# Performance work log

Hardware: AMD Instinct MI355X
Metric: run time of the kernel (lower is better)

The kernel has to match this reference:

```python
import jax, jax.numpy as jnp
import numpy as np

N, E, D, H = 50000, 800000, 128, 8
DH = D // H
EPS = 1e-12


def setup_inputs() -> dict:
    key = jax.random.key(0)
    ks = jax.random.split(key, 12)
    s = 0.02
    return {
        "h": jax.random.normal(ks[0], (N, D), jnp.float32),
        "Wq": jax.random.normal(ks[1], (D, D), jnp.float32) * s,
        "bq": jax.random.normal(ks[2], (D,), jnp.float32) * s,
        "Wk": jax.random.normal(ks[3], (D, D), jnp.float32) * s,
        "bk": jax.random.normal(ks[4], (D,), jnp.float32) * s,
        "Wv": jax.random.normal(ks[5], (D, D), jnp.float32) * s,
        "bv": jax.random.normal(ks[6], (D,), jnp.float32) * s,
        "Wo": jax.random.normal(ks[7], (D, D), jnp.float32) * s,
        "bo": jax.random.normal(ks[8], (D,), jnp.float32) * s,
        "gamma": jnp.ones((D,), jnp.float32),
        "beta": jnp.zeros((D,), jnp.float32),
        "src": jax.random.randint(ks[9], (E,), 0, N, jnp.int32),
        "dst": jax.random.randint(ks[10], (E,), 0, N, jnp.int32),
    }


def reference(h, Wq, bq, Wk, bk, Wv, bv, Wo, bo, gamma, beta, src, dst):
    n = h.shape[0]
    # node-wise projections, split into heads: [N, H, DH]
    Q = (h @ Wq + bq).reshape(n, H, DH)
    K = (h @ Wk + bk).reshape(n, H, DH)
    V = (h @ Wv + bv).reshape(n, H, DH)
    # edge-wise scores: sum over head dim of K[src] * Q[dst] -> [E, H]
    scores = jnp.sum(K[src] * Q[dst], axis=-1)
    # edge softmax, normalized over incoming edges of each dst node
    m = jax.lax.stop_gradient(jax.ops.segment_max(scores, dst, num_segments=n))
    ex = jnp.exp(scores - m[dst])
    denom = jax.ops.segment_sum(ex, dst, num_segments=n)
    p = ex / denom[dst]  # [E, H]
    # weighted message + scatter-sum aggregate -> [N, H, DH]
    msg = V[src] * p[:, :, None]
    agg = jax.ops.segment_sum(msg, dst, num_segments=n).reshape(n, D)
    # BertSelfOutput: dense + residual + layernorm (dropout is identity in eval)
    y = agg @ Wo + bo + h
    mu = jnp.mean(y, axis=-1, keepdims=True)
    var = jnp.mean(jnp.square(y - mu), axis=-1, keepdims=True)
    out = (y - mu) / jnp.sqrt(var + EPS) * gamma + beta
    return out
```

## Files before the change

kernel.cpp:

```cpp
#include <hip/hip_runtime.h>
#include <hip/hip_bf16.h>
#include <math.h>

#define D 128
#define EPS 1e-12f
#define CPAD 16

typedef __attribute__((ext_vector_type(8))) short bf16x8;
typedef __attribute__((ext_vector_type(4))) float f32x4;
typedef __attribute__((ext_vector_type(2))) float f32x2;

__device__ __forceinline__ unsigned short f2bf(float f) {
    unsigned int u = __float_as_uint(f);
    return (unsigned short)((u + 0x7fffu + ((u >> 16) & 1u)) >> 16);
}
__device__ __forceinline__ float bf2f_lo(unsigned int packed) {
    return __uint_as_float(packed << 16);
}
__device__ __forceinline__ float bf2f_hi(unsigned int packed) {
    return __uint_as_float(packed & 0xffff0000u);
}
__device__ __forceinline__ unsigned char f2fp8(float f) {
    return (unsigned char)__builtin_amdgcn_cvt_pk_fp8_f32(f, f, 0, false);
}

__global__ __launch_bounds__(256) void prep_kernel(
    const float* __restrict__ Wq, const float* __restrict__ Wk,
    const float* __restrict__ Wv, const float* __restrict__ Wo,
    unsigned short* __restrict__ WT,
    const int* __restrict__ dst, int* __restrict__ counts,
    int* __restrict__ ticket, int E) {
    int bx = blockIdx.x;
    int tid = threadIdx.x;
    if (bx < 64) {
        __shared__ unsigned short tile[32][33];
        int m = bx >> 4;
        int t = bx & 15;
        const float* W = (m == 0) ? Wq : (m == 1) ? Wk : (m == 2) ? Wv : Wo;
        int r0 = (t & 3) * 32;
        int c0 = (t >> 2) * 32;
        int row = tid >> 3, c4 = (tid & 7) * 4;
        float4 v = *(const float4*)&W[(size_t)(r0 + row) * D + c0 + c4];
        tile[c4 + 0][row] = f2bf(v.x);
        tile[c4 + 1][row] = f2bf(v.y);
        tile[c4 + 2][row] = f2bf(v.z);
        tile[c4 + 3][row] = f2bf(v.w);
        __syncthreads();
        unsigned int lo = (unsigned int)tile[row][c4] | ((unsigned int)tile[row][c4 + 1] << 16);
        unsigned int hi = (unsigned int)tile[row][c4 + 2] | ((unsigned int)tile[row][c4 + 3] << 16);
        uint2 pk; pk.x = lo; pk.y = hi;
        int n = c0 + row;
        int ct = n >> 4, l15 = n & 15;
        int ks = t & 3;
        int quad = c4 >> 3;
        int j = c4 & 7;
        size_t off = (size_t)m * 16384 + (size_t)(((ct * 4 + ks) * 64) + quad * 16 + l15) * 8 + j;
        *(uint2*)&WT[off] = pk;
    } else {
        int e = ((bx - 64) * 256 + tid) * 4;
        if (e >= E) return;
        if (e + 3 < E) {
            int4 d4 = *(const int4*)&dst[e];
            int4 t4;
            t4.x = atomicAdd(&counts[d4.x * CPAD], 1);
            t4.y = atomicAdd(&counts[d4.y * CPAD], 1);
            t4.z = atomicAdd(&counts[d4.z * CPAD], 1);
            t4.w = atomicAdd(&counts[d4.w * CPAD], 1);
            *(int4*)&ticket[e] = t4;
        } else {
            for (int i = e; i < E; ++i) ticket[i] = atomicAdd(&counts[dst[i] * CPAD], 1);
        }
    }
}

__device__ __forceinline__ int block_incl_scan256(int v, int tid, int* wsum) {
    int lane = tid & 63;
    int wid = tid >> 6;
#pragma unroll
    for (int off = 1; off < 64; off <<= 1) {
        int t = __shfl_up(v, off, 64);
        if (lane >= off) v += t;
    }
    if (lane == 63) wsum[wid] = v;
    __syncthreads();
#pragma unroll
    for (int w = 0; w < 4; ++w)
        if (w < wid) v += wsum[w];
    return v;
}

__global__ void scan1_kernel(const int* __restrict__ counts, int* __restrict__ offsets,
                             int* __restrict__ chunksum, int n) {
    __shared__ int wsum[4];
    int tid = threadIdx.x;
    int i = blockIdx.x * 256 + tid;
    int v = (i < n) ? counts[i * CPAD] : 0;
    int incl = block_incl_scan256(v, tid, wsum);
    if (i < n) offsets[i + 1] = incl;
    if (tid == 255) chunksum[blockIdx.x] = incl;
}

__global__ void scan23_kernel(int* __restrict__ offsets, const int* __restrict__ chunksum, int n) {
    __shared__ int wsum[4];
    int bx = blockIdx.x, tid = threadIdx.x;
    int v = 0;
    for (int t = tid; t < bx; t += 256) v += chunksum[t];
#pragma unroll
    for (int off = 32; off >= 1; off >>= 1) v += __shfl_xor(v, off, 64);
    if ((tid & 63) == 0) wsum[tid >> 6] = v;
    __syncthreads();
    int base = wsum[0] + wsum[1] + wsum[2] + wsum[3];
    int i = bx * 256 + tid;
    if (i < n) {
        offsets[i + 1] += base;
        if (i == 0) offsets[0] = 0;
    }
}

__global__ __launch_bounds__(256) void fill_qkv_kernel(
    const int* __restrict__ dst, const int* __restrict__ src,
    const int* __restrict__ ticket, const int* __restrict__ offsets,
    int* __restrict__ psrc, int E, int e4blocks,
    const float* __restrict__ h, const unsigned short* __restrict__ WT,
    const float* __restrict__ bq, const float* __restrict__ bk, const float* __restrict__ bv,
    unsigned short* __restrict__ Qb, unsigned char* __restrict__ KV8, int n) {
    __shared__ __align__(16) unsigned short wt[16384];
    int bx = blockIdx.x;
    int tid = threadIdx.x;
    if (bx < e4blocks) {
        int e = (bx * 256 + tid) * 4;
        if (e >= E) return;
        if (e + 3 < E) {
            int4 d4 = *(const int4*)&dst[e];
            int4 s4 = *(const int4*)&src[e];
            int4 t4 = *(const int4*)&ticket[e];
            psrc[offsets[d4.x] + t4.x] = s4.x;
            psrc[offsets[d4.y] + t4.y] = s4.y;
            psrc[offsets[d4.z] + t4.z] = s4.z;
            psrc[offsets[d4.w] + t4.w] = s4.w;
        } else {
            for (int i = e; i < E; ++i) psrc[offsets[dst[i]] + ticket[i]] = src[i];
        }
        return;
    }
    int bid = bx - e4blocks;
    int lane = tid & 63, wave = tid >> 6;
    int quad = lane >> 4, l15 = lane & 15;
    int rt = bid * 64 + wave * 16;

    int rowA = min(rt + l15, n - 1);
    bf16x8 af[4];
#pragma unroll
    for (int ks = 0; ks < 4; ++ks) {
        const float* ap = &h[(size_t)rowA * D + ks * 32 + quad * 8];
        float4 a0 = *(const float4*)ap;
        float4 a1 = *(const float4*)(ap + 4);
        union { unsigned short u[8]; bf16x8 v; } pk;
        pk.u[0] = f2bf(a0.x); pk.u[1] = f2bf(a0.y);
        pk.u[2] = f2bf(a0.z); pk.u[3] = f2bf(a0.w);
        pk.u[4] = f2bf(a1.x); pk.u[5] = f2bf(a1.y);
        pk.u[6] = f2bf(a1.z); pk.u[7] = f2bf(a1.w);
        af[ks] = pk.v;
    }

    for (int m = 0; m < 3; ++m) {
#pragma unroll
        for (int it = 0; it < 8; ++it) {
            int idx = it * 256 + tid;
            *(uint4*)&wt[idx * 8] = *(const uint4*)&WT[(size_t)m * 16384 + idx * 8];
        }
        __syncthreads();

        f32x4 acc[8];
#pragma unroll
        for (int ct = 0; ct < 8; ++ct) {
            acc[ct] = (f32x4){0.f, 0.f, 0.f, 0.f};
#pragma unroll
            for (int ks = 0; ks < 4; ++ks) {
                bf16x8 bfr = *(const bf16x8*)&wt[((ct * 4 + ks) * 64 + lane) * 8];
                acc[ct] = __builtin_amdgcn_mfma_f32_16x16x32_bf16(af[ks], bfr, acc[ct], 0, 0, 0);
            }
        }
        __syncthreads();

        const float* bias = (m == 0) ? bq : (m == 1) ? bk : bv;
#pragma unroll
        for (int ct = 0; ct < 8; ++ct) {
            int col = ct * 16 + l15;
            float bb = bias[col];
#pragma unroll
            for (int r = 0; r < 4; ++r) {
                int row = rt + quad * 4 + r;
                if (row < n) {
                    float v = acc[ct][r] + bb;
                    if (m == 0)      Qb[(size_t)row * D + col] = f2bf(v);
                    else if (m == 1) KV8[(size_t)row * 256 + col] = f2fp8(v);
                    else             KV8[(size_t)row * 256 + 128 + col] = f2fp8(v);
                }
            }
        }
    }
}

__global__ __launch_bounds__(256) void edge_attn_kernel(
    const unsigned short* __restrict__ Qb, const unsigned char* __restrict__ KV8,
    const int* __restrict__ offsets, const int* __restrict__ psrc,
    unsigned short* __restrict__ aggb, int n) {
    int node = (blockIdx.x * 256 + threadIdx.x) >> 5;
    int l32 = threadIdx.x & 31;
    if (node >= n) return;
    int start = offsets[node], end = offsets[node + 1];
    int j = l32 >> 3, hd = l32 & 7;

    const unsigned short* qp = &Qb[(size_t)node * D + hd * 16];
    uint4 qa = *(const uint4*)qp;
    uint4 qb = *(const uint4*)(qp + 8);
    float q[16];
    q[0] = bf2f_lo(qa.x);  q[1] = bf2f_hi(qa.x);
    q[2] = bf2f_lo(qa.y);  q[3] = bf2f_hi(qa.y);
    q[4] = bf2f_lo(qa.z);  q[5] = bf2f_hi(qa.z);
    q[6] = bf2f_lo(qa.w);  q[7] = bf2f_hi(qa.w);
    q[8] = bf2f_lo(qb.x);  q[9] = bf2f_hi(qb.x);
    q[10] = bf2f_lo(qb.y); q[11] = bf2f_hi(qb.y);
    q[12] = bf2f_lo(qb.z); q[13] = bf2f_hi(qb.z);
    q[14] = bf2f_lo(qb.w); q[15] = bf2f_hi(qb.w);

    float l = 0.f;
    float acc[16] = {};

    if (start < end) {
        int s = psrc[min(start + j, end - 1)];
        for (int base = start; base < end; base += 4) {
            const unsigned char* kvp = &KV8[(size_t)s * 256 + hd * 16];
            uint4 ku = *(const uint4*)kvp;
            uint4 vu = *(const uint4*)(kvp + 128);
            int nb = base + 4;
            int sn = (nb < end) ? psrc[min(nb + j, end - 1)] : 0;
            bool valid = (base + j) < end;

            float kf[16], vf[16];
            {
                f32x2 t;
                t = __builtin_amdgcn_cvt_pk_f32_fp8(ku.x, false); kf[0] = t.x;  kf[1] = t.y;
                t = __builtin_amdgcn_cvt_pk_f32_fp8(ku.x, true);  kf[2] = t.x;  kf[3] = t.y;
                t = __builtin_amdgcn_cvt_pk_f32_fp8(ku.y, false); kf[4] = t.x;  kf[5] = t.y;
                t = __builtin_amdgcn_cvt_pk_f32_fp8(ku.y, true);  kf[6] = t.x;  kf[7] = t.y;
                t = __builtin_amdgcn_cvt_pk_f32_fp8(ku.z, false); kf[8] = t.x;  kf[9] = t.y;
                t = __builtin_amdgcn_cvt_pk_f32_fp8(ku.z, true);  kf[10] = t.x; kf[11] = t.y;
                t = __builtin_amdgcn_cvt_pk_f32_fp8(ku.w, false); kf[12] = t.x; kf[13] = t.y;
                t = __builtin_amdgcn_cvt_pk_f32_fp8(ku.w, true);  kf[14] = t.x; kf[15] = t.y;
                t = __builtin_amdgcn_cvt_pk_f32_fp8(vu.x, false); vf[0] = t.x;  vf[1] = t.y;
                t = __builtin_amdgcn_cvt_pk_f32_fp8(vu.x, true);  vf[2] = t.x;  vf[3] = t.y;
                t = __builtin_amdgcn_cvt_pk_f32_fp8(vu.y, false); vf[4] = t.x;  vf[5] = t.y;
                t = __builtin_amdgcn_cvt_pk_f32_fp8(vu.y, true);  vf[6] = t.x;  vf[7] = t.y;
                t = __builtin_amdgcn_cvt_pk_f32_fp8(vu.z, false); vf[8] = t.x;  vf[9] = t.y;
                t = __builtin_amdgcn_cvt_pk_f32_fp8(vu.z, true);  vf[10] = t.x; vf[11] = t.y;
                t = __builtin_amdgcn_cvt_pk_f32_fp8(vu.w, false); vf[12] = t.x; vf[13] = t.y;
                t = __builtin_amdgcn_cvt_pk_f32_fp8(vu.w, true);  vf[14] = t.x; vf[15] = t.y;
            }

            float sc = q[0] * kf[0];
#pragma unroll
            for (int i = 1; i < 16; ++i) sc = fmaf(q[i], kf[i], sc);

            float p = valid ? __expf(sc) : 0.f;
            l += p;
#pragma unroll
            for (int i = 0; i < 16; ++i) acc[i] = fmaf(p, vf[i], acc[i]);
            s = sn;
        }
    }

#pragma unroll
    for (int off = 8; off <= 16; off <<= 1) {
        l += __shfl_xor(l, off, 64);
#pragma unroll
        for (int i = 0; i < 16; ++i) acc[i] += __shfl_xor(acc[i], off, 64);
    }
    float inv = (l > 0.f) ? 1.f / l : 0.f;
    if (j == 0) {
        uint4 o0, o1;
        o0.x = (unsigned int)f2bf(acc[0] * inv) | ((unsigned int)f2bf(acc[1] * inv) << 16);
        o0.y = (unsigned int)f2bf(acc[2] * inv) | ((unsigned int)f2bf(acc[3] * inv) << 16);
        o0.z = (unsigned int)f2bf(acc[4] * inv) | ((unsigned int)f2bf(acc[5] * inv) << 16);
        o0.w = (unsigned int)f2bf(acc[6] * inv) | ((unsigned int)f2bf(acc[7] * inv) << 16);
        o1.x = (unsigned int)f2bf(acc[8] * inv) | ((unsigned int)f2bf(acc[9] * inv) << 16);
        o1.y = (unsigned int)f2bf(acc[10] * inv) | ((unsigned int)f2bf(acc[11] * inv) << 16);
        o1.z = (unsigned int)f2bf(acc[12] * inv) | ((unsigned int)f2bf(acc[13] * inv) << 16);
        o1.w = (unsigned int)f2bf(acc[14] * inv) | ((unsigned int)f2bf(acc[15] * inv) << 16);
        unsigned short* op = &aggb[(size_t)node * D + hd * 16];
        *(uint4*)op = o0;
        *(uint4*)(op + 8) = o1;
    }
}

__global__ __launch_bounds__(256) void out_ln_mfma_kernel(
    const unsigned short* __restrict__ aggb, const unsigned short* __restrict__ WTo,
    const float* __restrict__ bo, const float* __restrict__ hres,
    const float* __restrict__ gamma, const float* __restrict__ beta,
    float* __restrict__ out, int n) {
    int tid = threadIdx.x;
    int lane = tid & 63, wave = tid >> 6;
    int quad = lane >> 4, l15 = lane & 15;
    int rt = blockIdx.x * 64 + wave * 16;

    int rowA = min(rt + l15, n - 1);
    bf16x8 af[4];
#pragma unroll
    for (int ks = 0; ks < 4; ++ks)
        af[ks] = *(const bf16x8*)&aggb[(size_t)rowA * D + ks * 32 + quad * 8];

    f32x4 acc[8];
#pragma unroll
    for (int ct = 0; ct < 8; ++ct) {
        acc[ct] = (f32x4){0.f, 0.f, 0.f, 0.f};
#pragma unroll
        for (int ks = 0; ks < 4; ++ks) {
            bf16x8 bfr = *(const bf16x8*)&WTo[(size_t)((ct * 4 + ks) * 64 + lane) * 8];
            acc[ct] = __builtin_amdgcn_mfma_f32_16x16x32_bf16(af[ks], bfr, acc[ct], 0, 0, 0);
        }
    }

    float bb[8], gg[8], be[8];
#pragma unroll
    for (int ct = 0; ct < 8; ++ct) {
        int col = ct * 16 + l15;
        bb[ct] = bo[col];
        gg[ct] = gamma[col];
        be[ct] = beta[col];
    }
#pragma unroll
    for (int ct = 0; ct < 8; ++ct) {
        int col = ct * 16 + l15;
#pragma unroll
        for (int r = 0; r < 4; ++r) {
            int row = rt + quad * 4 + r;
            float hv = (row < n) ? hres[(size_t)row * D + col] : 0.f;
            acc[ct][r] = acc[ct][r] + bb[ct] + hv;
        }
    }

#pragma unroll
    for (int r = 0; r < 4; ++r) {
        float s1 = 0.f, s2 = 0.f;
#pragma unroll
        for (int ct = 0; ct < 8; ++ct) {
            float v = acc[ct][r];
            s1 += v;
            s2 += v * v;
        }
        s1 += __shfl_xor(s1, 1, 64); s2 += __shfl_xor(s2, 1, 64);
        s1 += __shfl_xor(s1, 2, 64); s2 += __shfl_xor(s2, 2, 64);
        s1 += __shfl_xor(s1, 4, 64); s2 += __shfl_xor(s2, 4, 64);
        s1 += __shfl_xor(s1, 8, 64); s2 += __shfl_xor(s2, 8, 64);
        float mu = s1 * (1.f / 128.f);
        float var = s2 * (1.f / 128.f) - mu * mu;
        float rs = rsqrtf(fmaxf(var, 0.f) + EPS);
        int row = rt + quad * 4 + r;
        if (row < n) {
#pragma unroll
            for (int ct = 0; ct < 8; ++ct) {
                int col = ct * 16 + l15;
                out[(size_t)row * D + col] = (acc[ct][r] - mu) * rs * gg[ct] + be[ct];
            }
        }
    }
}

extern "C" void kernel_launch(void* const* d_in, const int* in_sizes, int n_in,
                              void* d_out, int out_size, void* d_ws, size_t ws_size,
                              hipStream_t stream) {
    const float* h     = (const float*)d_in[0];
    const float* Wq    = (const float*)d_in[1];
    const float* bq    = (const float*)d_in[2];
    const float* Wk    = (const float*)d_in[3];
    const float* bk    = (const float*)d_in[4];
    const float* Wv    = (const float*)d_in[5];
    const float* bv    = (const float*)d_in[6];
    const float* Wo    = (const float*)d_in[7];
    const float* bo    = (const float*)d_in[8];
    const float* gamma = (const float*)d_in[9];
    const float* beta  = (const float*)d_in[10];
    const int* src     = (const int*)d_in[11];
    const int* dst     = (const int*)d_in[12];
    float* out = (float*)d_out;

    int N = in_sizes[0] / D;
    int E = in_sizes[11];

    unsigned short* Qb = (unsigned short*)d_ws;
    unsigned short* Ab = Qb + (size_t)N * D;
    unsigned short* WT = Ab + (size_t)N * D;
    unsigned char* KV8 = (unsigned char*)(WT + 4 * D * D);
    int* counts   = (int*)(KV8 + (size_t)N * 256);
    int* offsets  = counts + (size_t)N * CPAD;
    int* chunksum = offsets + (N + 1);
    int* ticket   = chunksum + 256;
    int* psrc     = ticket + E;

    int nchunks = (N + 255) / 256;
    int e4blocks = ((E + 3) / 4 + 255) / 256;
    int nqkv = (N + 63) / 64;

    hipMemsetAsync(counts, 0, (size_t)N * CPAD * sizeof(int), stream);
    prep_kernel<<<64 + e4blocks, 256, 0, stream>>>(Wq, Wk, Wv, Wo, WT, dst, counts, ticket, E);
    scan1_kernel<<<nchunks, 256, 0, stream>>>(counts, offsets, chunksum, N);
    scan23_kernel<<<nchunks, 256, 0, stream>>>(offsets, chunksum, N);
    fill_qkv_kernel<<<e4blocks + nqkv, 256, 0, stream>>>(
        dst, src, ticket, offsets, psrc, E, e4blocks,
        h, WT, bq, bk, bv, Qb, KV8, N);
    edge_attn_kernel<<<(N + 7) / 8, 256, 0, stream>>>(Qb, KV8, offsets, psrc, Ab, N);
    out_ln_mfma_kernel<<<(N + 63) / 64, 256, 0, stream>>>(Ab, WT + 3 * D * D, bo, h, gamma, beta, out, N);
}
```

Before: 219.7 us.

## Fuse scan into single-pass decoupled kernel, double rows per QKV block, deepen edge prefetch

Merges the two scan kernels into one single-pass scan. Each block publishes its aggregate with a release flag, and later blocks spin-wait on the flags of earlier blocks. The QKV projection now computes 128 rows per block so each staged weight tile is reused across two row groups. The edge-attention loop prefetches KV data one iteration ahead and source indices two ahead. Together these are meant to cut a kernel launch, weight reload traffic, and gather latency, at the cost of spin-wait deadlock risk if blocks are not co-resident and higher register pressure.

After: 232.9 us. 6.0% more time.

```diff
diff --git a/kernel.cpp b/kernel.cpp
--- a/kernel.cpp
+++ b/kernel.cpp
@@ -73,9 +73,14 @@
     }
 }
 
-__device__ __forceinline__ int block_incl_scan256(int v, int tid, int* wsum) {
-    int lane = tid & 63;
-    int wid = tid >> 6;
+__global__ __launch_bounds__(256) void scan_kernel(
+    const int* __restrict__ counts, int* __restrict__ offsets,
+    int* __restrict__ agg, int* __restrict__ flag, int n) {
+    __shared__ int wsum[4];
+    int bx = blockIdx.x, tid = threadIdx.x;
+    int i = bx * 256 + tid;
+    int v = (i < n) ? counts[i * CPAD] : 0;
+    int lane = tid & 63, wid = tid >> 6;
 #pragma unroll
     for (int off = 1; off < 64; off <<= 1) {
         int t = __shfl_up(v, off, 64);
@@ -83,38 +88,27 @@
     }
     if (lane == 63) wsum[wid] = v;
     __syncthreads();
+    int incl = v;
 #pragma unroll
     for (int w = 0; w < 4; ++w)
-        if (w < wid) v += wsum[w];
-    return v;
-}
-
-__global__ void scan1_kernel(const int* __restrict__ counts, int* __restrict__ offsets,
-                             int* __restrict__ chunksum, int n) {
-    __shared__ int wsum[4];
-    int tid = threadIdx.x;
-    int i = blockIdx.x * 256 + tid;
-    int v = (i < n) ? counts[i * CPAD] : 0;
-    int incl = block_incl_scan256(v, tid, wsum);
-    if (i < n) offsets[i + 1] = incl;
-    if (tid == 255) chunksum[blockIdx.x] = incl;
-}
-
-__global__ void scan23_kernel(int* __restrict__ offsets, const int* __restrict__ chunksum, int n) {
-    __shared__ int wsum[4];
-    int bx = blockIdx.x, tid = threadIdx.x;
-    int v = 0;
-    for (int t = tid; t < bx; t += 256) v += chunksum[t];
-#pragma unroll
-    for (int off = 32; off >= 1; off >>= 1) v += __shfl_xor(v, off, 64);
-    if ((tid & 63) == 0) wsum[tid >> 6] = v;
+        if (w < wid) incl += wsum[w];
+    if (tid == 255) {
+        __hip_atomic_store(&agg[bx], incl, __ATOMIC_RELEASE, __HIP_MEMORY_SCOPE_AGENT);
+        __hip_atomic_store(&flag[bx], 1, __ATOMIC_RELEASE, __HIP_MEMORY_SCOPE_AGENT);
+    }
+    int p = 0;
+    for (int t = tid; t < bx; t += 256) {
+        while (__hip_atomic_load(&flag[t], __ATOMIC_ACQUIRE, __HIP_MEMORY_SCOPE_AGENT) == 0) {}
+        p += __hip_atomic_load(&agg[t], __ATOMIC_RELAXED, __HIP_MEMORY_SCOPE_AGENT);
+    }
+#pragma unroll
+    for (int off = 32; off >= 1; off >>= 1) p += __shfl_xor(p, off, 64);
+    __syncthreads();
+    if (lane == 0) wsum[wid] = p;
     __syncthreads();
     int base = wsum[0] + wsum[1] + wsum[2] + wsum[3];
-    int i = bx * 256 + tid;
-    if (i < n) {
-        offsets[i + 1] += base;
-        if (i == 0) offsets[0] = 0;
-    }
+    if (i < n) offsets[i + 1] = incl + base;
+    if (i == 0) offsets[0] = 0;
 }
 
 __global__ __launch_bounds__(256) void fill_qkv_kernel(
@@ -146,21 +140,24 @@
     int bid = bx - e4blocks;
     int lane = tid & 63, wave = tid >> 6;
     int quad = lane >> 4, l15 = lane & 15;
-    int rt = bid * 64 + wave * 16;
-
-    int rowA = min(rt + l15, n - 1);
-    bf16x8 af[4];
-#pragma unroll
-    for (int ks = 0; ks < 4; ++ks) {
-        const float* ap = &h[(size_t)rowA * D + ks * 32 + quad * 8];
-        float4 a0 = *(const float4*)ap;
-        float4 a1 = *(const float4*)(ap + 4);
-        union { unsigned short u[8]; bf16x8 v; } pk;
-        pk.u[0] = f2bf(a0.x); pk.u[1] = f2bf(a0.y);
-        pk.u[2] = f2bf(a0.z); pk.u[3] = f2bf(a0.w);
-        pk.u[4] = f2bf(a1.x); pk.u[5] = f2bf(a1.y);
-        pk.u[6] = f2bf(a1.z); pk.u[7] = f2bf(a1.w);
-        af[ks] = pk.v;
+    int rt0 = bid * 128 + wave * 16;
+
+    bf16x8 af[2][4];
+#pragma unroll
+    for (int hh = 0; hh < 2; ++hh) {
+        int rowA = min(rt0 + hh * 64 + l15, n - 1);
+#pragma unroll
+        for (int ks = 0; ks < 4; ++ks) {
+            const float* ap = &h[(size_t)rowA * D + ks * 32 + quad * 8];
+            float4 a0 = *(const float4*)ap;
+            float4 a1 = *(const float4*)(ap + 4);
+            union { unsigned short u[8]; bf16x8 v; } pk;
+            pk.u[0] = f2bf(a0.x); pk.u[1] = f2bf(a0.y);
+            pk.u[2] = f2bf(a0.z); pk.u[3] = f2bf(a0.w);
+            pk.u[4] = f2bf(a1.x); pk.u[5] = f2bf(a1.y);
+            pk.u[6] = f2bf(a1.z); pk.u[7] = f2bf(a1.w);
+            af[hh][ks] = pk.v;
+        }
     }
 
     for (int m = 0; m < 3; ++m) {
@@ -171,34 +168,37 @@
         }
         __syncthreads();
 
-        f32x4 acc[8];
-#pragma unroll
-        for (int ct = 0; ct < 8; ++ct) {
-            acc[ct] = (f32x4){0.f, 0.f, 0.f, 0.f};
-#pragma unroll
-            for (int ks = 0; ks < 4; ++ks) {
-                bf16x8 bfr = *(const bf16x8*)&wt[((ct * 4 + ks) * 64 + lane) * 8];
-                acc[ct] = __builtin_amdgcn_mfma_f32_16x16x32_bf16(af[ks], bfr, acc[ct], 0, 0, 0);
-            }
-        }
-        __syncthreads();
-
         const float* bias = (m == 0) ? bq : (m == 1) ? bk : bv;
 #pragma unroll
-        for (int ct = 0; ct < 8; ++ct) {
-            int col = ct * 16 + l15;
-            float bb = bias[col];
-#pragma unroll
-            for (int r = 0; r < 4; ++r) {
-                int row = rt + quad * 4 + r;
-                if (row < n) {
-                    float v = acc[ct][r] + bb;
-                    if (m == 0)      Qb[(size_t)row * D + col] = f2bf(v);
-                    else if (m == 1) KV8[(size_t)row * 256 + col] = f2fp8(v);
-                    else             KV8[(size_t)row * 256 + 128 + col] = f2fp8(v);
+        for (int hh = 0; hh < 2; ++hh) {
+            int rt = rt0 + hh * 64;
+            f32x4 acc[8];
+#pragma unroll
+            for (int ct = 0; ct < 8; ++ct) {
+                acc[ct] = (f32x4){0.f, 0.f, 0.f, 0.f};
+#pragma unroll
+                for (int ks = 0; ks < 4; ++ks) {
+                    bf16x8 bfr = *(const bf16x8*)&wt[((ct * 4 + ks) * 64 + lane) * 8];
+                    acc[ct] = __builtin_amdgcn_mfma_f32_16x16x32_bf16(af[hh][ks], bfr, acc[ct], 0, 0, 0);
                 }
             }
-        }
+#pragma unroll
+            for (int ct = 0; ct < 8; ++ct) {
+                int col = ct * 16 + l15;
+                float bb = bias[col];
+#pragma unroll
+                for (int r = 0; r < 4; ++r) {
+                    int row = rt + quad * 4 + r;
+                    if (row < n) {
+                        float v = acc[ct][r] + bb;
+                        if (m == 0)      Qb[(size_t)row * D + col] = f2bf(v);
+                        else if (m == 1) KV8[(size_t)row * 256 + col] = f2fp8(v);
+                        else             KV8[(size_t)row * 256 + 128 + col] = f2fp8(v);
+                    }
+                }
+            }
+        }
+        __syncthreads();
     }
 }
 
@@ -229,13 +229,16 @@
     float acc[16] = {};
 
     if (start < end) {
-        int s = psrc[min(start + j, end - 1)];
+        int s0 = psrc[min(start + j, end - 1)];
+        int s1 = (start + 4 < end) ? psrc[min(start + 4 + j, end - 1)] : 0;
+        const unsigned char* kvp = &KV8[(size_t)s0 * 256 + hd * 16];
+        uint4 ku = *(const uint4*)kvp;
+        uint4 vu = *(const uint4*)(kvp + 128);
         for (int base = start; base < end; base += 4) {
-            const unsigned char* kvp = &KV8[(size_t)s * 256 + hd * 16];
-            uint4 ku = *(const uint4*)kvp;
-            uint4 vu = *(const uint4*)(kvp + 128);
-            int nb = base + 4;
-            int sn = (nb < end) ? psrc[min(nb + j, end - 1)] : 0;
+            const unsigned char* kvpn = &KV8[(size_t)s1 * 256 + hd * 16];
+            uint4 kun = *(const uint4*)kvpn;
+            uint4 vun = *(const uint4*)(kvpn + 128);
+            int s2 = (base + 8 < end) ? psrc[min(base + 8 + j, end - 1)] : 0;
             bool valid = (base + j) < end;
 
             float kf[16], vf[16];
@@ -267,7 +270,7 @@
             l += p;
 #pragma unroll
             for (int i = 0; i < 16; ++i) acc[i] = fmaf(p, vf[i], acc[i]);
-            s = sn;
+            ku = kun; vu = vun; s1 = s2;
         }
     }
 
@@ -393,19 +396,19 @@
     unsigned short* WT = Ab + (size_t)N * D;
     unsigned char* KV8 = (unsigned char*)(WT + 4 * D * D);
     int* counts   = (int*)(KV8 + (size_t)N * 256);
-    int* offsets  = counts + (size_t)N * CPAD;
-    int* chunksum = offsets + (N + 1);
-    int* ticket   = chunksum + 256;
+    int* flagarr  = counts + (size_t)N * CPAD;
+    int* offsets  = flagarr + 256;
+    int* agg      = offsets + (N + 1);
+    int* ticket   = agg + 256;
     int* psrc     = ticket + E;
 
     int nchunks = (N + 255) / 256;
     int e4blocks = ((E + 3) / 4 + 255) / 256;
-    int nqkv = (N + 63) / 64;
-
-    hipMemsetAsync(counts, 0, (size_t)N * CPAD * sizeof(int), stream);
+    int nqkv = (N + 127) / 128;
+
+    hipMemsetAsync(counts, 0, ((size_t)N * CPAD + 256) * sizeof(int), stream);
     prep_kernel<<<64 + e4blocks, 256, 0, stream>>>(Wq, Wk, Wv, Wo, WT, dst, counts, ticket, E);
-    scan1_kernel<<<nchunks, 256, 0, stream>>>(counts, offsets, chunksum, N);
-    scan23_kernel<<<nchunks, 256, 0, stream>>>(offsets, chunksum, N);
+    scan_kernel<<<nchunks, 256, 0, stream>>>(counts, offsets, agg, flagarr, N);
     fill_qkv_kernel<<<e4blocks + nqkv, 256, 0, stream>>>(
         dst, src, ticket, offsets, psrc, E, e4blocks,
         h, WT, bq, bk, bv, Qb, KV8, N);
```
